# Kernel tuning notes

Measured on AMD Instinct MI355X. Metric: run time of the kernel, lower is better.

The kernel has to match this reference:

```python
import jax, jax.numpy as jnp
import numpy as np

# Static config (matches init_kwargs)
B = 1
D = 1024          # model_dim
H = 16            # num_heads
HD = 64           # head_dim
TPF = 256         # tokens_per_frame = latent_height*latent_width
LH, LW = 16, 16
FRAMES = 13
PREFIX = 1
ATTN = 3
CHUNKS = 4
TXT = 226                 # text_length per chunk
SEQ_TXT = CHUNKS * TXT    # 904
VID_LEN = FRAMES * TPF    # 3328
CHUNK_VID = (PREFIX + ATTN) * TPF  # 1024 video tokens per attention chunk
THETA = 10000.0
EPS = 1e-6
SCALE = 1.0 / np.sqrt(HD)
DT, DHE, DW = 16, 24, 24  # 3D rope split of head_dim


def setup_inputs() -> dict:
    key = jax.random.key(0)
    ks = jax.random.split(key, 16)
    def w(k, shape, s=0.02):
        return (jax.random.normal(k, shape) * s).astype(jnp.float32)
    return dict(
        vid_emb=jax.random.normal(ks[0], (B, VID_LEN, D), jnp.float32),
        text_emb=jax.random.normal(ks[1], (B, SEQ_TXT, D), jnp.float32),
        Wq=w(ks[2], (D, D)), bq=jnp.zeros((D,), jnp.float32),
        Wk=w(ks[3], (D, D)), bk=jnp.zeros((D,), jnp.float32),
        Wv=w(ks[4], (D, D)), bv=jnp.zeros((D,), jnp.float32),
        Wo=w(ks[5], (D, D)), bo=jnp.zeros((D,), jnp.float32),
        qn_w=jnp.ones((HD,), jnp.float32), qn_b=jnp.zeros((HD,), jnp.float32),
        kn_w=jnp.ones((HD,), jnp.float32), kn_b=jnp.zeros((HD,), jnp.float32),
        ssm_Win=w(ks[6], (D, D)), ssm_Wout=w(ks[7], (D, D)),
        ssm_gate=jnp.zeros((D,), jnp.float32),
        fg_t=jnp.full((D,), 0.1, jnp.float32), fg_v=jnp.full((D,), 0.1, jnp.float32),
        bg_t=jnp.full((D,), 0.1, jnp.float32), bg_v=jnp.full((D,), 0.1, jnp.float32),
    )


def _layernorm(x, w, b):
    mu = jnp.mean(x, axis=-1, keepdims=True)
    var = jnp.mean((x - mu) ** 2, axis=-1, keepdims=True)
    return (x - mu) * jax.lax.rsqrt(var + EPS) * w + b


def _rope_angles():
    # per-video-token 3D positions within a chunk
    tok = jnp.arange(CHUNK_VID)
    f = (tok // TPF).astype(jnp.float32)
    rem = tok % TPF
    hp = (rem // LW).astype(jnp.float32)
    wp = (rem % LW).astype(jnp.float32)
    def inv(d):
        return THETA ** (-jnp.arange(0, d, 2, dtype=jnp.float32) / d)
    return f[:, None] * inv(DT), hp[:, None] * inv(DHE), wp[:, None] * inv(DW)


def _rot(x, ang):
    half = x.shape[-1] // 2
    c, s = jnp.cos(ang), jnp.sin(ang)
    x1, x2 = x[..., :half], x[..., half:]
    return jnp.concatenate([x1 * c - x2 * s, x1 * s + x2 * c], axis=-1)


def _apply_rope3d(x, angs):
    at, ah, aw = angs
    return jnp.concatenate([
        _rot(x[..., :DT], at),
        _rot(x[..., DT:DT + DHE], ah),
        _rot(x[..., DT + DHE:], aw),
    ], axis=-1)


def _attn_forward(vid_emb, text_emb, Wq, bq, Wk, bk, Wv, bv, Wo, bo, qn_w, qn_b, kn_w, kn_b):
    b = vid_emb.shape[0]
    starts = np.arange(CHUNKS) * ATTN * TPF
    idx = jnp.asarray(starts)[:, None] + jnp.arange(CHUNK_VID)[None, :]  # [C, CHUNK_VID]
    txt_chunks = text_emb.reshape(b, CHUNKS, TXT, D)
    vid_chunks = vid_emb[:, idx]                                          # [b, C, CHUNK_VID, D]
    cur = jnp.concatenate([txt_chunks, vid_chunks], axis=2)               # [b, C, T, D]
    T = TXT + CHUNK_VID
    cur = cur.reshape(b * CHUNKS, T, D)

    def heads(x):
        return x.reshape(b * CHUNKS, T, H, HD).transpose(0, 2, 1, 3)      # [bc, h, t, d]

    q = _layernorm(heads(cur @ Wq + bq), qn_w, qn_b)
    k = _layernorm(heads(cur @ Wk + bk), kn_w, kn_b)
    v = heads(cur @ Wv + bv)

    angs = _rope_angles()
    q = jnp.concatenate([q[:, :, :TXT], _apply_rope3d(q[:, :, TXT:], angs)], axis=2)
    k = jnp.concatenate([k[:, :, :TXT], _apply_rope3d(k[:, :, TXT:], angs)], axis=2)

    scores = jnp.einsum('bhqd,bhkd->bhqk', q, k) * SCALE
    attn = jax.nn.softmax(scores, axis=-1)
    out = jnp.einsum('bhqk,bhkd->bhqd', attn, v)
    out = out.transpose(0, 2, 1, 3).reshape(b * CHUNKS, T, D) @ Wo + bo
    out = out.reshape(b, CHUNKS, T, D)

    text_out = out[:, :, :TXT].reshape(b, SEQ_TXT, D)
    vid_part = out[:, :, TXT:]                                            # [b, C, CHUNK_VID, D]
    vid_acc = jnp.zeros((b, VID_LEN, D), vid_emb.dtype).at[:, idx].add(vid_part)
    cnt = jnp.zeros((b, VID_LEN, 1), vid_emb.dtype).at[:, idx].add(jnp.ones((b, CHUNKS, CHUNK_VID, 1), vid_emb.dtype))
    vid_out = vid_acc / cnt
    return jnp.concatenate([text_out, vid_out], axis=1)


def _ssm(x, Win, Wout, gate_logit):
    # simplified TTT stand-in: gated linear recurrence h_t = g*h_{t-1} + u_t (causal scan)
    g = jax.nn.sigmoid(gate_logit)
    u = x @ Win
    a = jnp.broadcast_to(g, u.shape)
    def comb(c1, c2):
        a1, b1 = c1
        a2, b2 = c2
        return a1 * a2, a2 * b1 + b2
    _, h = jax.lax.associative_scan(comb, (a, u), axis=1)
    return h @ Wout


def _rev_text_chunks(t):
    b = t.shape[0]
    return jnp.flip(t.reshape(b, CHUNKS, TXT, D), axis=1).reshape(b, SEQ_TXT, D)


def _ssm_forward(emb, ssm_Win, ssm_Wout, ssm_gate, fg_t, fg_v, bg_t, bg_v):
    Ttxt = SEQ_TXT
    res = emb
    y = _ssm(emb, ssm_Win, ssm_Wout, ssm_gate)
    emb = res + jnp.concatenate([jnp.tanh(fg_t) * y[:, :Ttxt], jnp.tanh(fg_v) * y[:, Ttxt:]], axis=1)
    res2 = emb
    # multiscene reverse: flip text chunk order and video token order
    rev = jnp.concatenate([_rev_text_chunks(emb[:, :Ttxt]), jnp.flip(emb[:, Ttxt:], axis=1)], axis=1)
    y2 = _ssm(rev, ssm_Win, ssm_Wout, ssm_gate)
    y2 = jnp.concatenate([_rev_text_chunks(y2[:, :Ttxt]), jnp.flip(y2[:, Ttxt:], axis=1)], axis=1)
    return res2 + jnp.concatenate([jnp.tanh(bg_t) * y2[:, :Ttxt], jnp.tanh(bg_v) * y2[:, Ttxt:]], axis=1)


def reference(vid_emb, text_emb, Wq, bq, Wk, bk, Wv, bv, Wo, bo, qn_w, qn_b, kn_w, kn_b,
              ssm_Win, ssm_Wout, ssm_gate, fg_t, fg_v, bg_t, bg_v):
    emb = _attn_forward(vid_emb, text_emb, Wq, bq, Wk, bk, Wv, bv, Wo, bo, qn_w, qn_b, kn_w, kn_b)
    out = _ssm_forward(emb, ssm_Win, ssm_Wout, ssm_gate, fg_t, fg_v, bg_t, bg_v)
    return out[:, SEQ_TXT:], out[:, :SEQ_TXT]
```

## Files before the change

### kernel.cpp

```cpp
#include <hip/hip_runtime.h>
#include <cstdint>

constexpr int Dm       = 1024;
constexpr int Hh       = 16;
constexpr int HD       = 64;
constexpr int CHUNKS   = 4;
constexpr int TXT      = 226;
constexpr int SEQ_TXT  = 904;
constexpr int VID_LEN  = 3328;
constexpr int CHUNK_VID= 1024;
constexpr int Tt       = 1250;
constexpr int Tp       = 1280;
constexpr int M_QKV    = 5000;
constexpr int SEQm     = 4232;
constexpr int STRIDE_V = 768;
constexpr float EPSc   = 1e-6f;
constexpr float SCALEc = 0.125f;
constexpr float OFFS   = 8.0f;
constexpr float C16    = 1.6609640474f;
constexpr float C24    = 1.1073093649f;

constexpr int SEGL2 = 64;
constexpr int HALO  = 64;
constexpr int NSEG2 = (SEQm + SEGL2 - 1) / SEGL2;

typedef __attribute__((ext_vector_type(8))) short bf16x8;
typedef __attribute__((ext_vector_type(4))) float f32x4;

__device__ __forceinline__ ushort f2bf(float x) {
    uint32_t u = __float_as_uint(x);
    u += 0x7FFFu + ((u >> 16) & 1u);
    return (ushort)(u >> 16);
}
__device__ __forceinline__ float bf2f(ushort b) {
    return __uint_as_float(((uint32_t)b) << 16);
}

__device__ __forceinline__ void gload_lds16(const ushort* g, ushort* l) {
    __builtin_amdgcn_global_load_lds(
        (const __attribute__((address_space(1))) unsigned int*)g,
        (__attribute__((address_space(3))) unsigned int*)l, 16, 0, 0);
}

__device__ __forceinline__ int rev_map(int i) {
    if (i < SEQ_TXT) {
        int c = i / TXT, o = i - c * TXT;
        return (CHUNKS - 1 - c) * TXT + o;
    }
    int j = i - SEQ_TXT;
    return SEQ_TXT + (VID_LEN - 1 - j);
}

__global__ __launch_bounds__(256) void prep_all(
    const float* __restrict__ Wq, const float* __restrict__ Wk,
    const float* __restrict__ Wv, const float* __restrict__ Wo,
    const float* __restrict__ Win, const float* __restrict__ Wout,
    const float* __restrict__ vid, const float* __restrict__ txt,
    ushort* __restrict__ WqkvH, ushort* __restrict__ WqkvL,
    ushort* __restrict__ WoH, ushort* __restrict__ WoL,
    ushort* __restrict__ WinH, ushort* __restrict__ WinL,
    ushort* __restrict__ WoutH, ushort* __restrict__ WoutL,
    ushort* __restrict__ chi, ushort* __restrict__ clo) {
    __shared__ float tile[32][33];
    if (blockIdx.z == 6) {
        int base = (blockIdx.y * 32 + blockIdx.x) * 256 + threadIdx.x;
        for (int idx = base; idx < M_QKV * 256; idx += 32 * 32 * 256) {
            int row = idx >> 8, c4 = (idx & 255) * 4;
            int c = row / Tt, t = row - c * Tt;
            float4 x;
            if (t < TXT)
                x = *(const float4*)(txt + (size_t)(c * TXT + t) * Dm + c4);
            else
                x = *(const float4*)(vid + (size_t)(c * STRIDE_V + (t - TXT)) * Dm + c4);
            float v[4] = {x.x, x.y, x.z, x.w};
            ushort4 h, l;
            h.x = f2bf(v[0]); l.x = f2bf(v[0] - bf2f(h.x));
            h.y = f2bf(v[1]); l.y = f2bf(v[1] - bf2f(h.y));
            h.z = f2bf(v[2]); l.z = f2bf(v[2] - bf2f(h.z));
            h.w = f2bf(v[3]); l.w = f2bf(v[3] - bf2f(h.w));
            *(ushort4*)(chi + (size_t)row * Dm + c4) = h;
            *(ushort4*)(clo + (size_t)row * Dm + c4) = l;
        }
        return;
    }
    const float* W; ushort* Thi; ushort* Tlo;
    switch (blockIdx.z) {
        case 0: W = Wq;  Thi = WqkvH;               Tlo = WqkvL;               break;
        case 1: W = Wk;  Thi = WqkvH + 1024*1024;   Tlo = WqkvL + 1024*1024;   break;
        case 2: W = Wv;  Thi = WqkvH + 2*1024*1024; Tlo = WqkvL + 2*1024*1024; break;
        case 3: W = Wo;  Thi = WoH;   Tlo = WoL;   break;
        case 4: W = Win; Thi = WinH;  Tlo = WinL;  break;
        default:W = Wout;Thi = WoutH; Tlo = WoutL; break;
    }
    int k0 = blockIdx.y * 32, n0 = blockIdx.x * 32;
    int j = threadIdx.x & 31, i0 = threadIdx.x >> 5;
#pragma unroll
    for (int i = i0; i < 32; i += 8)
        tile[i][j] = W[(size_t)(k0 + i) * 1024 + n0 + j];
    __syncthreads();
#pragma unroll
    for (int i = i0; i < 32; i += 8) {
        float v = tile[j][i];
        ushort h = f2bf(v);
        size_t o = (size_t)(n0 + i) * 1024 + k0 + j;
        Thi[o] = h;
        Tlo[o] = f2bf(v - bf2f(h));
    }
}

__global__ __launch_bounds__(256) void gemm_fk(
    const ushort* __restrict__ Ahi, const ushort* __restrict__ Alo,
    const ushort* __restrict__ Bhi, const ushort* __restrict__ Blo,
    float* __restrict__ Cf, int M, int N) {
    __shared__ ushort AHL[2][128 * 64];
    __shared__ ushort BHL[2][64 * 64];
    const int tid = threadIdx.x;
    const int w = tid >> 6, lane = tid & 63;
    const int lrow = lane & 15, quad = lane >> 4;
    const int mBase = blockIdx.y * 128, nBase = blockIdx.x * 64;

    const int srow = tid >> 3;
    const int cch  = (tid & 7) ^ (srow & 7);
    const ushort* PA = (cch < 4) ? Ahi : Alo;
    const ushort* PB = (cch < 4) ? Bhi : Blo;
    uint32_t gA[4], gB[2];
#pragma unroll
    for (int q = 0; q < 4; ++q)
        gA[q] = (uint32_t)(min(mBase + q * 32 + srow, M - 1) * 1024 + (cch & 3) * 8);
#pragma unroll
    for (int q = 0; q < 2; ++q)
        gB[q] = (uint32_t)((nBase + q * 32 + srow) * 1024 + (cch & 3) * 8);
    const int ldsW = w * 512;

    const int wm = w >> 1, wn = w & 1;
    const int p = quad ^ (lrow & 7);
    const int arow = wm * 64 + lrow;
    const int brow = wn * 32 + lrow;

    f32x4 acc[4][2];
#pragma unroll
    for (int i = 0; i < 4; ++i)
#pragma unroll
        for (int j = 0; j < 2; ++j) acc[i][j] = (f32x4){0.f, 0.f, 0.f, 0.f};

#define STAGE_FK(buf, kk) do { \
        gload_lds16(PA + gA[0] + (kk), &AHL[buf][0 * 2048 + ldsW]); \
        gload_lds16(PA + gA[1] + (kk), &AHL[buf][1 * 2048 + ldsW]); \
        gload_lds16(PA + gA[2] + (kk), &AHL[buf][2 * 2048 + ldsW]); \
        gload_lds16(PA + gA[3] + (kk), &AHL[buf][3 * 2048 + ldsW]); \
        gload_lds16(PB + gB[0] + (kk), &BHL[buf][0 * 2048 + ldsW]); \
        gload_lds16(PB + gB[1] + (kk), &BHL[buf][1 * 2048 + ldsW]); \
    } while (0)

    STAGE_FK(0, 0);
    asm volatile("s_waitcnt vmcnt(0)" ::: "memory");
    __builtin_amdgcn_s_barrier();

    int it = 0;
    for (int kk = 0; kk < 1024; kk += 32, ++it) {
        const int b = it & 1;
        if (kk + 32 < 1024) STAGE_FK(1 - b, kk + 32);

        bf16x8 ah[4], al[4], bh[2], bl[2];
#pragma unroll
        for (int i = 0; i < 4; ++i) {
            const ushort* rp = &AHL[b][(arow + i * 16) * 64];
            ah[i] = *(const bf16x8*)(rp + p * 8);
            al[i] = *(const bf16x8*)(rp + (p ^ 4) * 8);
        }
#pragma unroll
        for (int j = 0; j < 2; ++j) {
            const ushort* rp = &BHL[b][(brow + j * 16) * 64];
            bh[j] = *(const bf16x8*)(rp + p * 8);
            bl[j] = *(const bf16x8*)(rp + (p ^ 4) * 8);
        }
        __builtin_amdgcn_s_setprio(1);
#pragma unroll
        for (int i = 0; i < 4; ++i)
#pragma unroll
            for (int j = 0; j < 2; ++j) {
                f32x4 a = acc[i][j];
                a = __builtin_amdgcn_mfma_f32_16x16x32_bf16(ah[i], bh[j], a, 0, 0, 0);
                a = __builtin_amdgcn_mfma_f32_16x16x32_bf16(al[i], bh[j], a, 0, 0, 0);
                a = __builtin_amdgcn_mfma_f32_16x16x32_bf16(ah[i], bl[j], a, 0, 0, 0);
                acc[i][j] = a;
            }
        __builtin_amdgcn_s_setprio(0);
        asm volatile("s_waitcnt vmcnt(0)" ::: "memory");
        __builtin_amdgcn_s_barrier();
    }
#undef STAGE_FK

#pragma unroll
    for (int i = 0; i < 4; ++i)
#pragma unroll
        for (int j = 0; j < 2; ++j) {
            const int col = nBase + wn * 32 + j * 16 + lrow;
#pragma unroll
            for (int r = 0; r < 4; ++r) {
                const int row = mBase + wm * 64 + i * 16 + quad * 4 + r;
                if (row < M) Cf[(size_t)row * N + col] = acc[i][j][r];
            }
        }
}

__global__ __launch_bounds__(512, 2) void gemm_qkv_8ph(
    const ushort* __restrict__ Ahi, const ushort* __restrict__ Alo,
    const ushort* __restrict__ Bhi, const ushort* __restrict__ Blo,
    const float* __restrict__ f1, const float* __restrict__ f2,
    const float* __restrict__ f3, ushort* __restrict__ out) {
    constexpr int Mq  = M_QKV;
    constexpr int Nq  = 3072;
    constexpr int NSL = 32;

    __shared__ __align__(16) ushort ldsq[65536];

    const int tid = threadIdx.x;
    const int w = tid >> 6, lane = tid & 63;
    const int lrow = lane & 15, quad = lane >> 4;
    const int wr = w >> 2, wc = w & 3;
    const int mBase = blockIdx.y * 256, nBase = blockIdx.x * 256;

    const int cA = (tid & 7) ^ ((tid >> 3) & 7);
    const ushort* pA = (cA < 4) ? Ahi : Alo;
    const ushort* pB = (cA < 4) ? Bhi : Blo;
    uint32_t offA[4], offB[4];
#pragma unroll
    for (int q = 0; q < 4; ++q) {
        const int r = q * 64 + (tid >> 3);
        offA[q] = (uint32_t)(min(mBase + r, Mq - 1) * 1024 + (cA & 3) * 8);
        offB[q] = (uint32_t)((nBase + r) * 1024 + (cA & 3) * 8);
    }
    const int ldsW = w * 512;

    const int pH = quad ^ (lrow & 7);
    const int arow = wr * 128 + lrow;
    const int brow = wc * 64 + lrow;

    f32x4 acc[8][4];
#pragma unroll
    for (int i = 0; i < 8; ++i)
#pragma unroll
        for (int j = 0; j < 4; ++j) acc[i][j] = (f32x4){0.f, 0.f, 0.f, 0.f};

#define STAGE_AB(b, s) do { \
        ushort* dA_ = ldsq + (b) * 16384 + ldsW; \
        ushort* dB_ = ldsq + 32768 + (b) * 16384 + ldsW; \
        const uint32_t ko_ = (uint32_t)(s) * 32u; \
        gload_lds16(pA + offA[0] + ko_, dA_); \
        gload_lds16(pA + offA[1] + ko_, dA_ + 4096); \
        gload_lds16(pA + offA[2] + ko_, dA_ + 8192); \
        gload_lds16(pA + offA[3] + ko_, dA_ + 12288); \
        gload_lds16(pB + offB[0] + ko_, dB_); \
        gload_lds16(pB + offB[1] + ko_, dB_ + 4096); \
        gload_lds16(pB + offB[2] + ko_, dB_ + 8192); \
        gload_lds16(pB + offB[3] + ko_, dB_ + 12288); \
    } while (0)

    STAGE_AB(0, 0);
    asm volatile("s_waitcnt vmcnt(0)" ::: "memory");
    __builtin_amdgcn_s_barrier();

#pragma unroll 1
    for (int s = 0; s < NSL; ++s) {
        const int b = s & 1;
        if (s + 1 < NSL) STAGE_AB(1 - b, s + 1);

        const ushort* aB_ = ldsq + b * 16384;
        const ushort* bB_ = ldsq + 32768 + b * 16384;
        bf16x8 ahi[8], alo[8], bhi[4], blo[4];
#pragma unroll
        for (int i = 0; i < 8; ++i) {
            const ushort* rp = aB_ + (arow + i * 16) * 64;
            ahi[i] = *(const bf16x8*)(rp + pH * 8);
            alo[i] = *(const bf16x8*)(rp + (pH ^ 4) * 8);
        }
#pragma unroll
        for (int j = 0; j < 4; ++j) {
            const ushort* rp = bB_ + (brow + j * 16) * 64;
            bhi[j] = *(const bf16x8*)(rp + pH * 8);
            blo[j] = *(const bf16x8*)(rp + (pH ^ 4) * 8);
        }

        __builtin_amdgcn_s_barrier();
        asm volatile("s_waitcnt lgkmcnt(0)" ::: "memory");
        __builtin_amdgcn_s_setprio(1);
#pragma unroll
        for (int i = 0; i < 8; ++i)
#pragma unroll
            for (int j = 0; j < 4; ++j) {
                f32x4 a = acc[i][j];
                a = __builtin_amdgcn_mfma_f32_16x16x32_bf16(ahi[i], bhi[j], a, 0, 0, 0);
                a = __builtin_amdgcn_mfma_f32_16x16x32_bf16(alo[i], bhi[j], a, 0, 0, 0);
                a = __builtin_amdgcn_mfma_f32_16x16x32_bf16(ahi[i], blo[j], a, 0, 0, 0);
                acc[i][j] = a;
            }
        __builtin_amdgcn_s_setprio(0);
        asm volatile("s_waitcnt vmcnt(0)" ::: "memory");
        __builtin_amdgcn_s_barrier();
    }

#undef STAGE_AB

#pragma unroll
    for (int i = 0; i < 8; ++i) {
#pragma unroll
        for (int j = 0; j < 4; ++j) {
            const int col = nBase + wc * 64 + j * 16 + lrow;
            const float bias = (col < 1024) ? f1[col]
                             : (col < 2048) ? f2[col - 1024] : f3[col - 2048];
#pragma unroll
            for (int r = 0; r < 4; ++r) {
                const int row = mBase + wr * 128 + i * 16 + quad * 4 + r;
                if (row < Mq)
                    out[(size_t)row * Nq + col] = f2bf(acc[i][j][r] + bias);
            }
        }
    }
}

__global__ __launch_bounds__(256) void lnrope(
    const ushort* __restrict__ qkvb,
    const float* __restrict__ qn_w, const float* __restrict__ qn_b,
    const float* __restrict__ kn_w, const float* __restrict__ kn_b,
    ushort* __restrict__ qP, ushort* __restrict__ kP, ushort* __restrict__ vT) {
    __shared__ ushort vtile[64][72];
    const int ch = blockIdx.y, c = ch >> 4, h = ch & 15;
    const int t0 = blockIdx.x * 64;
    const int tid = threadIdx.x, w = tid >> 6, lane = tid & 63;

    auto wsum = [](float x) {
#pragma unroll
        for (int o = 32; o; o >>= 1) x += __shfl_xor(x, o);
        return x;
    };

#pragma unroll 1
    for (int it = 0; it < 16; ++it) {
        const int tl = w * 16 + it;
        const int t = t0 + tl;
        ushort qb = 0, kb = 0, vb = 0;
        if (t < Tt) {
            size_t src = (size_t)(c * Tt + t) * 3072 + h * HD + lane;
            float qv = bf2f(qkvb[src]);
            float kv = bf2f(qkvb[src + 1024]);
            float vv = bf2f(qkvb[src + 2048]);

            float qmu = wsum(qv) * (1.f / 64.f);
            float qd  = qv - qmu;
            float qvar = wsum(qd * qd) * (1.f / 64.f);
            float qn = qd * rsqrtf(qvar + EPSc) * qn_w[lane] + qn_b[lane];

            float kmu = wsum(kv) * (1.f / 64.f);
            float kd  = kv - kmu;
            float kvar = wsum(kd * kd) * (1.f / 64.f);
            float kn = kd * rsqrtf(kvar + EPSc) * kn_w[lane] + kn_b[lane];

            if (t >= TXT) {
                int pos = t - TXT;
                int f = pos >> 8, rem2 = pos & 255, hp = rem2 >> 4, wp = rem2 & 15;
                int p, dl; float cc;
                if (lane < 16)      { cc = C16; p = f;  dl = lane; }
                else if (lane < 40) { cc = C24; p = hp; dl = lane - 16; }
                else                { cc = C24; p = wp; dl = lane - 40; }
                int halfd = (lane < 16) ? 8 : 12;
                int i = (dl < halfd) ? dl : dl - halfd;
                float ang = (float)p * exp2f(-(float)i * cc);
                float cs = cosf(ang), sn = sinf(ang);
                int partner = (dl < halfd) ? (lane + halfd) : (lane - halfd);
                float qo = __shfl(qn, partner);
                float ko = __shfl(kn, partner);
                qn = (dl < halfd) ? (qn * cs - qo * sn) : (qo * sn + qn * cs);
                kn = (dl < halfd) ? (kn * cs - ko * sn) : (ko * sn + kn * cs);
            }
            qb = f2bf(qn * SCALEc);
            kb = f2bf(kn);
            vb = f2bf(vv);
        }
        size_t dst = ((size_t)ch * Tp + t) * HD + lane;
        qP[dst] = qb;
        kP[dst] = kb;
        vtile[tl][lane] = vb;
    }
    __syncthreads();
    const int r = tid >> 2, ck = tid & 3;
    ushort* dst = vT + ((size_t)ch * HD + r) * Tp + t0;
    short o1[8], o2[8];
#pragma unroll
    for (int j = 0; j < 8; ++j) {
        o1[j] = (short)vtile[ck * 8 + j][r];
        o2[j] = (short)vtile[(ck + 4) * 8 + j][r];
    }
    *(bf16x8*)(dst + ck * 8)       = *(bf16x8*)o1;
    *(bf16x8*)(dst + (ck + 4) * 8) = *(bf16x8*)o2;
}

__global__ __launch_bounds__(256) void attn_mfma(
    const ushort* __restrict__ qP, const ushort* __restrict__ kP,
    const ushort* __restrict__ vT,
    ushort* __restrict__ ohi, ushort* __restrict__ olo) {
    const int ch = blockIdx.y;
    const int c = ch >> 4, h = ch & 15;
    const int qbase = blockIdx.x * 64;
    const int tid = threadIdx.x, w = tid >> 6, lane = tid & 63;
    const int lrow = lane & 15, quad = lane >> 4;

    __shared__ ushort KT[2][32 * 64];
    __shared__ ushort VTs[2][64 * 32];
    __shared__ ushort PB[4][16][40];

    const ushort* kg = kP + (size_t)ch * Tp * HD;
    const ushort* vg = vT + (size_t)ch * HD * Tp;

    const ushort* kgl = kg + (size_t)(w * 8 + (lane >> 3)) * HD
                           + ((lane & 7) ^ ((lane >> 3) & 7)) * 8;
    const ushort* vgl = vg + (size_t)(w * 16 + (lane >> 2)) * Tp + (lane & 3) * 8;

    const int qr = qbase + w * 16 + lrow;
    const ushort* qgp = qP + ((size_t)ch * Tp + qr) * HD + quad * 8;
    bf16x8 qf0 = *(const bf16x8*)qgp;
    bf16x8 qf1 = *(const bf16x8*)(qgp + 32);

    f32x4 accO[4];
#pragma unroll
    for (int dt = 0; dt < 4; ++dt) accO[dt] = (f32x4){0.f, 0.f, 0.f, 0.f};
    float lacc[4] = {0.f, 0.f, 0.f, 0.f};

    gload_lds16(kgl, &KT[0][w * 512]);
    gload_lds16(vgl, &VTs[0][w * 512]);

    const int NSTEP = Tp / 32;
    for (int s = 0; s < NSTEP; ++s) {
        const int b = s & 1;
        __syncthreads();
        if (s + 1 < NSTEP) {
            int kb = (s + 1) * 32;
            gload_lds16(kgl + (size_t)kb * HD, &KT[1 - b][w * 512]);
            gload_lds16(vgl + kb, &VTs[1 - b][w * 512]);
        }

        const int sw = lrow & 7;
        const ushort* r0 = &KT[b][lrow * 64];
        const ushort* r1 = &KT[b][(16 + lrow) * 64];
        bf16x8 k00 = *(const bf16x8*)(r0 + (quad ^ sw) * 8);
        bf16x8 k01 = *(const bf16x8*)(r0 + ((4 + quad) ^ sw) * 8);
        bf16x8 k10 = *(const bf16x8*)(r1 + (quad ^ sw) * 8);
        bf16x8 k11 = *(const bf16x8*)(r1 + ((4 + quad) ^ sw) * 8);
        f32x4 s0 = (f32x4){0.f, 0.f, 0.f, 0.f}, s1 = s0;
        s0 = __builtin_amdgcn_mfma_f32_16x16x32_bf16(qf0, k00, s0, 0, 0, 0);
        s0 = __builtin_amdgcn_mfma_f32_16x16x32_bf16(qf1, k01, s0, 0, 0, 0);
        s1 = __builtin_amdgcn_mfma_f32_16x16x32_bf16(qf0, k10, s1, 0, 0, 0);
        s1 = __builtin_amdgcn_mfma_f32_16x16x32_bf16(qf1, k11, s1, 0, 0, 0);

#pragma unroll
        for (int r = 0; r < 4; ++r) {
            float p0 = __expf(s0[r] - OFFS);
            float p1 = __expf(s1[r] - OFFS);
            lacc[r] += p0 + p1;
            int row = quad * 4 + r;
            PB[w][row][lrow]      = f2bf(p0);
            PB[w][row][16 + lrow] = f2bf(p1);
        }

        bf16x8 pf = *(const bf16x8*)&PB[w][lrow][quad * 8];
#pragma unroll
        for (int dt = 0; dt < 4; ++dt) {
            bf16x8 vf = *(const bf16x8*)&VTs[b][(dt * 16 + lrow) * 32 + quad * 8];
            accO[dt] = __builtin_amdgcn_mfma_f32_16x16x32_bf16(pf, vf, accO[dt], 0, 0, 0);
        }
    }

    float il[4];
#pragma unroll
    for (int r = 0; r < 4; ++r) {
        float l = lacc[r];
        l += __shfl_xor(l, 1);
        l += __shfl_xor(l, 2);
        l += __shfl_xor(l, 4);
        l += __shfl_xor(l, 8);
        l -= (float)(Tp - Tt) * __expf(-OFFS);
        il[r] = 1.f / l;
    }
#pragma unroll
    for (int dt = 0; dt < 4; ++dt)
#pragma unroll
        for (int r = 0; r < 4; ++r) {
            int qrow = qbase + w * 16 + quad * 4 + r;
            if (qrow < Tt) {
                float val = accO[dt][r] * il[r];
                size_t o = (size_t)(c * Tt + qrow) * Dm + h * HD + dt * 16 + lrow;
                ushort hv = f2bf(val);
                ohi[o] = hv;
                olo[o] = f2bf(val - bf2f(hv));
            }
        }
}

__global__ __launch_bounds__(256) void reduce_scatter(
    const float* __restrict__ P0, const float* __restrict__ bo,
    ushort* __restrict__ ehi, ushort* __restrict__ elo) {
    int idx = blockIdx.x * 256 + threadIdx.x;
    int row = idx >> 8, c4 = (idx & 255) * 4;
    float sx, sy, sz, sw;
    if (row < SEQ_TXT) {
        int c = row / TXT, t = row - c * TXT;
        size_t o = (size_t)(c * Tt + t) * Dm + c4;
        float4 a = *(const float4*)(P0 + o);
        sx = a.x; sy = a.y; sz = a.z; sw = a.w;
    } else {
        int p = row - SEQ_TXT;
        sx = sy = sz = sw = 0.f; int cnt = 0;
#pragma unroll
        for (int c = 0; c < CHUNKS; ++c) {
            int off = p - c * STRIDE_V;
            if (off >= 0 && off < CHUNK_VID) {
                size_t o = (size_t)(c * Tt + TXT + off) * Dm + c4;
                float4 a = *(const float4*)(P0 + o);
                sx += a.x; sy += a.y; sz += a.z; sw += a.w;
                ++cnt;
            }
        }
        float inv = 1.f / (float)cnt;
        sx *= inv; sy *= inv; sz *= inv; sw *= inv;
    }
    float4 b4 = *(const float4*)(bo + c4);
    float v[4] = {sx + b4.x, sy + b4.y, sz + b4.z, sw + b4.w};
    ushort4 h, l;
    h.x = f2bf(v[0]); l.x = f2bf(v[0] - bf2f(h.x));
    h.y = f2bf(v[1]); l.y = f2bf(v[1] - bf2f(h.y));
    h.z = f2bf(v[2]); l.z = f2bf(v[2] - bf2f(h.z));
    h.w = f2bf(v[3]); l.w = f2bf(v[3] - bf2f(h.w));
    *(ushort4*)(ehi + (size_t)row * Dm + c4) = h;
    *(ushort4*)(elo + (size_t)row * Dm + c4) = l;
}

__global__ __launch_bounds__(256) void scan_halo(
    const float* __restrict__ P0, const float* __restrict__ gate,
    ushort* __restrict__ hhi, ushort* __restrict__ hlo, int perm) {
    int ch = blockIdx.x * 256 + threadIdx.x;
    int seg = blockIdx.y;
    float g = 1.f / (1.f + expf(-gate[ch]));
    int tw0 = seg * SEGL2;
    int tw1 = min(SEQm, tw0 + SEGL2);
    int t0 = max(0, tw0 - HALO);
    float hv = 0.f;
    for (int t = t0; t < tw0; ++t) {
        int rt = perm ? rev_map(t) : t;
        hv = fmaf(g, hv, P0[(size_t)rt * Dm + ch]);
    }
    for (int t = tw0; t < tw1; ++t) {
        int rt = perm ? rev_map(t) : t;
        size_t o = (size_t)rt * Dm + ch;
        hv = fmaf(g, hv, P0[o]);
        ushort h = f2bf(hv);
        hhi[o] = h;
        hlo[o] = f2bf(hv - bf2f(h));
    }
}

__global__ __launch_bounds__(256) void reduce_c1(
    const float* __restrict__ P0,
    const ushort* __restrict__ ehi, const ushort* __restrict__ elo,
    const float* __restrict__ fg_t, const float* __restrict__ fg_v,
    float* __restrict__ emb2, ushort* __restrict__ e2hi, ushort* __restrict__ e2lo) {
    int idx = blockIdx.x * 256 + threadIdx.x;
    int row = idx >> 8, c4 = (idx & 255) * 4;
    const float* fg = (row < SEQ_TXT) ? fg_t : fg_v;
    size_t o = (size_t)row * Dm + c4;
    float4 a = *(const float4*)(P0 + o);
    ushort4 eh = *(const ushort4*)(ehi + o);
    ushort4 el = *(const ushort4*)(elo + o);
    float v[4];
    v[0] = (bf2f(eh.x) + bf2f(el.x)) + tanhf(fg[c4 + 0]) * a.x;
    v[1] = (bf2f(eh.y) + bf2f(el.y)) + tanhf(fg[c4 + 1]) * a.y;
    v[2] = (bf2f(eh.z) + bf2f(el.z)) + tanhf(fg[c4 + 2]) * a.z;
    v[3] = (bf2f(eh.w) + bf2f(el.w)) + tanhf(fg[c4 + 3]) * a.w;
    *(float4*)(emb2 + o) = make_float4(v[0], v[1], v[2], v[3]);
    ushort4 h, l;
    h.x = f2bf(v[0]); l.x = f2bf(v[0] - bf2f(h.x));
    h.y = f2bf(v[1]); l.y = f2bf(v[1] - bf2f(h.y));
    h.z = f2bf(v[2]); l.z = f2bf(v[2] - bf2f(h.z));
    h.w = f2bf(v[3]); l.w = f2bf(v[3] - bf2f(h.w));
    *(ushort4*)(e2hi + o) = h;
    *(ushort4*)(e2lo + o) = l;
}

__global__ __launch_bounds__(256) void reduce_fin(
    const float* __restrict__ P0, const float* __restrict__ emb2,
    const float* __restrict__ bg_t, const float* __restrict__ bg_v,
    float* __restrict__ outp) {
    int idx = blockIdx.x * 256 + threadIdx.x;
    int row = idx >> 8, c4 = (idx & 255) * 4;
    const float* bg = (row < SEQ_TXT) ? bg_t : bg_v;
    int drow = (row >= SEQ_TXT) ? (row - SEQ_TXT) : (VID_LEN + row);
    size_t o = (size_t)row * Dm + c4;
    float4 a = *(const float4*)(P0 + o);
    float4 e = *(const float4*)(emb2 + o);
    float4 r = make_float4(e.x + tanhf(bg[c4 + 0]) * a.x,
                           e.y + tanhf(bg[c4 + 1]) * a.y,
                           e.z + tanhf(bg[c4 + 2]) * a.z,
                           e.w + tanhf(bg[c4 + 3]) * a.w);
    *(float4*)(outp + (size_t)drow * Dm + c4) = r;
}

extern "C" void kernel_launch(void* const* d_in, const int* in_sizes, int n_in,
                              void* d_out, int out_size, void* d_ws, size_t ws_size,
                              hipStream_t stream) {
    const float* vid_emb = (const float*)d_in[0];
    const float* text_emb= (const float*)d_in[1];
    const float* Wq = (const float*)d_in[2];  const float* bq = (const float*)d_in[3];
    const float* Wk = (const float*)d_in[4];  const float* bk = (const float*)d_in[5];
    const float* Wv = (const float*)d_in[6];  const float* bv = (const float*)d_in[7];
    const float* Wo = (const float*)d_in[8];  const float* bo = (const float*)d_in[9];
    const float* qn_w = (const float*)d_in[10]; const float* qn_b = (const float*)d_in[11];
    const float* kn_w = (const float*)d_in[12]; const float* kn_b = (const float*)d_in[13];
    const float* Win  = (const float*)d_in[14]; const float* Wout = (const float*)d_in[15];
    const float* gate = (const float*)d_in[16];
    const float* fg_t = (const float*)d_in[17]; const float* fg_v = (const float*)d_in[18];
    const float* bg_t = (const float*)d_in[19]; const float* bg_v = (const float*)d_in[20];

    char* W8 = (char*)d_ws;
    if (ws_size < 128647168u) return;
    ushort* WqkvH = (ushort*)(W8 + 0);
    ushort* WqkvL = (ushort*)(W8 + 6291456);
    ushort* WoH   = (ushort*)(W8 + 12582912);
    ushort* WoL   = (ushort*)(W8 + 14680064);
    ushort* WinH  = (ushort*)(W8 + 16777216);
    ushort* WinL  = (ushort*)(W8 + 18874368);
    ushort* WoutH = (ushort*)(W8 + 20971520);
    ushort* WoutL = (ushort*)(W8 + 23068672);
    ushort* qkvb  = (ushort*)(W8 + 25165824);
    ushort* curH  = (ushort*)(W8 + 55885824);
    ushort* curL  = (ushort*)(W8 + 66125824);
    ushort* qPl   = (ushort*)(W8 + 76365824);
    ushort* kPl   = (ushort*)(W8 + 86851584);
    ushort* vTl   = (ushort*)(W8 + 97337344);
    ushort* aoutH = (ushort*)(W8 + 25165824);
    ushort* aoutL = (ushort*)(W8 + 35405824);
    float*  PWo   = (float*) (W8 + 76365824);
    ushort* embH  = (ushort*)(W8 + 45645824);
    ushort* embL  = (ushort*)(W8 + 54312960);
    float*  PW    = (float*) (W8 + 76365824);
    ushort* hbufH = (ushort*)(W8 + 25165824);
    ushort* hbufL = (ushort*)(W8 + 33832960);
    float*  emb2  = (float*) (W8 + 111034368);
    ushort* e2H   = (ushort*)(W8 + 25165824);
    ushort* e2L   = (ushort*)(W8 + 33832960);
    ushort* hbuf2H= (ushort*)(W8 + 45645824);
    ushort* hbuf2L= (ushort*)(W8 + 54312960);
    float*  outp  = (float*)d_out;

    prep_all<<<dim3(32, 32, 7), 256, 0, stream>>>(
        Wq, Wk, Wv, Wo, Win, Wout, vid_emb, text_emb,
        WqkvH, WqkvL, WoH, WoL, WinH, WinL, WoutH, WoutL, curH, curL);

    gemm_qkv_8ph<<<dim3(12, 20), 512, 0, stream>>>(
        curH, curL, WqkvH, WqkvL, bq, bk, bv, qkvb);

    lnrope<<<dim3(Tp / 64, 64), 256, 0, stream>>>(qkvb, qn_w, qn_b, kn_w, kn_b,
                                                  qPl, kPl, vTl);

    attn_mfma<<<dim3(Tp / 64, 64), 256, 0, stream>>>(qPl, kPl, vTl, aoutH, aoutL);

    gemm_fk<<<dim3(16, 40), 256, 0, stream>>>(
        aoutH, aoutL, WoH, WoL, PWo, M_QKV, 1024);
    reduce_scatter<<<SEQm, 256, 0, stream>>>(PWo, bo, embH, embL);

    dim3 gfk(16, 34);
    dim3 gscan(Dm / 256, NSEG2);

    gemm_fk<<<gfk, 256, 0, stream>>>(embH, embL, WinH, WinL, PW, SEQm, 1024);
    scan_halo<<<gscan, 256, 0, stream>>>(PW, gate, hbufH, hbufL, 0);
    gemm_fk<<<gfk, 256, 0, stream>>>(hbufH, hbufL, WoutH, WoutL, PW, SEQm, 1024);
    reduce_c1<<<SEQm, 256, 0, stream>>>(PW, embH, embL, fg_t, fg_v,
                                        emb2, e2H, e2L);

    gemm_fk<<<gfk, 256, 0, stream>>>(e2H, e2L, WinH, WinL, PW, SEQm, 1024);
    scan_halo<<<gscan, 256, 0, stream>>>(PW, gate, hbuf2H, hbuf2L, 1);
    gemm_fk<<<gfk, 256, 0, stream>>>(hbuf2H, hbuf2L, WoutH, WoutL, PW, SEQm, 1024);
    reduce_fin<<<SEQm, 256, 0, stream>>>(PW, emb2, bg_t, bg_v, outp);
}
```

Before: 647.7 us.

## Enlarge gemm_fk tile to 128x128 with warp-specialized A/B staging

Widens the split-bf16 GEMM block tile from 128x64 to 128x128, so each wave now computes a 64x64 sub-tile (4x4 MFMA accumulators). Two waves load the A tile and two load the B tile, each issuing eight async global-to-LDS loads. The aim is to raise the ratio of MFMA work to LDS and global traffic and to halve the number of blocks. The cost is more accumulator registers and twice the B tile in shared memory, which may lower occupancy. The grids for the GEMM launches shrink from 16 to 8 blocks along N.

```diff
diff --git a/kernel.cpp b/kernel.cpp
--- a/kernel.cpp
+++ b/kernel.cpp
@@ -113,72 +113,72 @@
     const ushort* __restrict__ Bhi, const ushort* __restrict__ Blo,
     float* __restrict__ Cf, int M, int N) {
     __shared__ ushort AHL[2][128 * 64];
-    __shared__ ushort BHL[2][64 * 64];
+    __shared__ ushort BHL[2][128 * 64];
     const int tid = threadIdx.x;
     const int w = tid >> 6, lane = tid & 63;
     const int lrow = lane & 15, quad = lane >> 4;
-    const int mBase = blockIdx.y * 128, nBase = blockIdx.x * 64;
-
-    const int srow = tid >> 3;
-    const int cch  = (tid & 7) ^ (srow & 7);
-    const ushort* PA = (cch < 4) ? Ahi : Alo;
-    const ushort* PB = (cch < 4) ? Bhi : Blo;
-    uint32_t gA[4], gB[2];
-#pragma unroll
-    for (int q = 0; q < 4; ++q)
-        gA[q] = (uint32_t)(min(mBase + q * 32 + srow, M - 1) * 1024 + (cch & 3) * 8);
-#pragma unroll
-    for (int q = 0; q < 2; ++q)
-        gB[q] = (uint32_t)((nBase + q * 32 + srow) * 1024 + (cch & 3) * 8);
-    const int ldsW = w * 512;
-
-    const int wm = w >> 1, wn = w & 1;
+    const int mBase = blockIdx.y * 128, nBase = blockIdx.x * 128;
+
+    const bool isB = (w >= 2);
+    const int half = w & 1;
+    const ushort* Phi = isB ? Bhi : Ahi;
+    const ushort* Plo = isB ? Blo : Alo;
+    ushort* st0 = (isB ? BHL[0] : AHL[0]) + half * 4096;
+    ushort* st1 = (isB ? BHL[1] : AHL[1]) + half * 4096;
+    const int baseR = (isB ? nBase : mBase) + half * 64;
+    const int maxr = (isB ? N : M) - 1;
+    const int rl8 = lane >> 3;
+    const int c = (lane & 7) ^ rl8;
+    const ushort* Psel = (c < 4) ? Phi : Plo;
+    const ushort* gb[8];
+#pragma unroll
+    for (int u = 0; u < 8; ++u) {
+        int rg = min(baseR + u * 8 + rl8, maxr);
+        gb[u] = Psel + (size_t)rg * 1024 + (c & 3) * 8;
+    }
+
+    const int mo = (w >> 1) * 64, no = (w & 1) * 64;
     const int p = quad ^ (lrow & 7);
-    const int arow = wm * 64 + lrow;
-    const int brow = wn * 32 + lrow;
-
-    f32x4 acc[4][2];
+    f32x4 acc[4][4];
 #pragma unroll
     for (int i = 0; i < 4; ++i)
 #pragma unroll
-        for (int j = 0; j < 2; ++j) acc[i][j] = (f32x4){0.f, 0.f, 0.f, 0.f};
-
-#define STAGE_FK(buf, kk) do { \
-        gload_lds16(PA + gA[0] + (kk), &AHL[buf][0 * 2048 + ldsW]); \
-        gload_lds16(PA + gA[1] + (kk), &AHL[buf][1 * 2048 + ldsW]); \
-        gload_lds16(PA + gA[2] + (kk), &AHL[buf][2 * 2048 + ldsW]); \
-        gload_lds16(PA + gA[3] + (kk), &AHL[buf][3 * 2048 + ldsW]); \
-        gload_lds16(PB + gB[0] + (kk), &BHL[buf][0 * 2048 + ldsW]); \
-        gload_lds16(PB + gB[1] + (kk), &BHL[buf][1 * 2048 + ldsW]); \
-    } while (0)
-
-    STAGE_FK(0, 0);
+        for (int j = 0; j < 4; ++j) acc[i][j] = (f32x4){0.f, 0.f, 0.f, 0.f};
+
+#pragma unroll
+    for (int u = 0; u < 8; ++u) gload_lds16(gb[u], st0 + u * 512);
     asm volatile("s_waitcnt vmcnt(0)" ::: "memory");
     __builtin_amdgcn_s_barrier();
 
     int it = 0;
     for (int kk = 0; kk < 1024; kk += 32, ++it) {
         const int b = it & 1;
-        if (kk + 32 < 1024) STAGE_FK(1 - b, kk + 32);
-
-        bf16x8 ah[4], al[4], bh[2], bl[2];
+        ushort* stN = b ? st0 : st1;
+        if (kk + 32 < 1024) {
+#pragma unroll
+            for (int u = 0; u < 8; ++u) gload_lds16(gb[u] + kk + 32, stN + u * 512);
+        }
+
+        const ushort* Ab = AHL[b];
+        const ushort* Bb = BHL[b];
+        bf16x8 ah[4], al[4], bh[4], bl[4];
 #pragma unroll
         for (int i = 0; i < 4; ++i) {
-            const ushort* rp = &AHL[b][(arow + i * 16) * 64];
-            ah[i] = *(const bf16x8*)(rp + p * 8);
-            al[i] = *(const bf16x8*)(rp + (p ^ 4) * 8);
-        }
-#pragma unroll
-        for (int j = 0; j < 2; ++j) {
-            const ushort* rp = &BHL[b][(brow + j * 16) * 64];
-            bh[j] = *(const bf16x8*)(rp + p * 8);
-            bl[j] = *(const bf16x8*)(rp + (p ^ 4) * 8);
+            int m = mo + i * 16 + lrow;
+            ah[i] = *(const bf16x8*)&Ab[m * 64 + p * 8];
+            al[i] = *(const bf16x8*)&Ab[m * 64 + (p ^ 4) * 8];
+        }
+#pragma unroll
+        for (int j = 0; j < 4; ++j) {
+            int n = no + j * 16 + lrow;
+            bh[j] = *(const bf16x8*)&Bb[n * 64 + p * 8];
+            bl[j] = *(const bf16x8*)&Bb[n * 64 + (p ^ 4) * 8];
         }
         __builtin_amdgcn_s_setprio(1);
 #pragma unroll
         for (int i = 0; i < 4; ++i)
 #pragma unroll
-            for (int j = 0; j < 2; ++j) {
+            for (int j = 0; j < 4; ++j) {
                 f32x4 a = acc[i][j];
                 a = __builtin_amdgcn_mfma_f32_16x16x32_bf16(ah[i], bh[j], a, 0, 0, 0);
                 a = __builtin_amdgcn_mfma_f32_16x16x32_bf16(al[i], bh[j], a, 0, 0, 0);
@@ -189,16 +189,15 @@
         asm volatile("s_waitcnt vmcnt(0)" ::: "memory");
         __builtin_amdgcn_s_barrier();
     }
-#undef STAGE_FK
 
 #pragma unroll
     for (int i = 0; i < 4; ++i)
 #pragma unroll
-        for (int j = 0; j < 2; ++j) {
-            const int col = nBase + wn * 32 + j * 16 + lrow;
+        for (int j = 0; j < 4; ++j) {
+            const int col = nBase + no + j * 16 + lrow;
 #pragma unroll
             for (int r = 0; r < 4; ++r) {
-                const int row = mBase + wm * 64 + i * 16 + quad * 4 + r;
+                const int row = mBase + mo + i * 16 + quad * 4 + r;
                 if (row < M) Cf[(size_t)row * N + col] = acc[i][j][r];
             }
         }
@@ -662,11 +661,11 @@
 
     attn_mfma<<<dim3(Tp / 64, 64), 256, 0, stream>>>(qPl, kPl, vTl, aoutH, aoutL);
 
-    gemm_fk<<<dim3(16, 40), 256, 0, stream>>>(
+    gemm_fk<<<dim3(8, 40), 256, 0, stream>>>(
         aoutH, aoutL, WoH, WoL, PWo, M_QKV, 1024);
     reduce_scatter<<<SEQm, 256, 0, stream>>>(PWo, bo, embH, embL);
 
-    dim3 gfk(16, 34);
+    dim3 gfk(8, 34);
     dim3 gscan(Dm / 256, NSEG2);
 
     gemm_fk<<<gfk, 256, 0, stream>>>(embH, embL, WinH, WinL, PW, SEQm, 1024);
```

New measurement: 651.5 us. No clear change (+0.6%).
